# Kernel tuning notes

Measured on AMD Instinct MI355X. Metric: run time of the kernel, lower is better.

The kernel has to match this reference:

```python
import jax, jax.numpy as jnp
import numpy as np

NUM_ROUTES = 12800   # 32 * 20 * 20
NUM_CAPS = 25
IN_CH = 8
OUT_CH = 64
BATCH = 8
NUM_ITERS = 3


def setup_inputs() -> dict:
    key = jax.random.key(0)
    kx, kw = jax.random.split(key)
    x = jax.random.normal(kx, (BATCH, NUM_ROUTES, IN_CH), dtype=jnp.float32)
    # W parameter: torch shape [1, R, C, O, I] -> store as [R, C, O, I]
    W = jax.random.normal(kw, (NUM_ROUTES, NUM_CAPS, OUT_CH, IN_CH), dtype=jnp.float32)
    return {"x": x, "W": W}


def _squash_elementwise(s):
    # Faithful to source: squared_norm sums over last dim of s_j which has size 1,
    # so squash acts elementwise: s^2 * s / ((1+s^2) * |s|) = s*|s|/(1+s^2).
    sq = s * s
    return sq * s / ((1.0 + sq) * jnp.sqrt(sq))


def reference(x, W):
    # u_hat[b,r,c,o] = sum_i W[r,c,o,i] * x[b,r,i]
    u_hat = jnp.einsum('rcoi,bri->brco', W, x)  # [B, R, C, O]
    b_ij = jnp.zeros((NUM_ROUTES, NUM_CAPS), dtype=x.dtype)
    v = None
    for it in range(NUM_ITERS):
        # legacy F.softmax on 4D [1,R,C,1] uses implicit dim=1 -> over routes
        c_ij = jax.nn.softmax(b_ij, axis=0)                  # [R, C]
        s = jnp.einsum('rc,brco->bco', c_ij, u_hat)          # [B, C, O]
        v = _squash_elementwise(s)
        if it < NUM_ITERS - 1:
            # agreement: <u_hat, v> per (b,r,c), then mean over batch
            a = jnp.einsum('brco,bco->brc', u_hat, v)
            b_ij = b_ij + jnp.mean(a, axis=0)
    # torch returns v_j.squeeze(1) with shape [B, C, O, 1]
    return v[..., None]
```

## Files before the change

kernel.cpp:

```cpp
#include <hip/hip_runtime.h>
#include <cstdint>
#include <cstddef>

#define RN 12800
#define CN 25
#define ON 64
#define IN_ 8
#define BN 8
#define SOUT (BN*CN*ON)

#define RPC 64
#define NRC (RN / RPC)

template<int MODE>
__global__ void __launch_bounds__(320, 6)
caps_pass(const float* __restrict__ x, const float* __restrict__ W,
          const float* __restrict__ vin, const float* __restrict__ bin,
          float* __restrict__ bout, float* __restrict__ Sp, float* __restrict__ Zp)
{
    __shared__ float xs[RPC][BN][IN_];

    const int chunk = blockIdx.y;
    const int r0 = chunk * RPC;

    for (int t = threadIdx.x; t < RPC * BN * 2; t += 320) {
        const int i4 = t & 1;
        const int rl = (t >> 1) & (RPC - 1);
        const int b  = t >> 7;
        const float4 val = *reinterpret_cast<const float4*>(
            x + (((size_t)b * RN + r0 + rl) * IN_) + i4 * 4);
        *reinterpret_cast<float4*>(&xs[rl][b][i4 * 4]) = val;
    }
    __syncthreads();

    const int wave = threadIdx.x >> 6;
    const int lane = threadIdx.x & 63;
    const int c = blockIdx.x * 5 + wave;

    float acc[BN];
    #pragma unroll
    for (int b = 0; b < BN; ++b) acc[b] = 0.f;

    float vreg[BN];
    if (MODE >= 1) {
        #pragma unroll
        for (int b = 0; b < BN; ++b)
            vreg[b] = vin[(b * CN + c) * ON + lane];
    }
    float zacc = 0.f;

    #pragma unroll 2
    for (int rl = 0; rl < RPC; ++rl) {
        const int r = r0 + rl;
        const float4* wp = reinterpret_cast<const float4*>(
            W + ((((size_t)r * CN + c) * ON + lane) * IN_));
        const float4 w0 = wp[0];
        const float4 w1 = wp[1];

        float u[BN];
        #pragma unroll
        for (int b = 0; b < BN; ++b) {
            const float4 xa = *reinterpret_cast<const float4*>(&xs[rl][b][0]);
            const float4 xb = *reinterpret_cast<const float4*>(&xs[rl][b][4]);
            u[b] = w0.x*xa.x + w0.y*xa.y + w0.z*xa.z + w0.w*xa.w
                 + w1.x*xb.x + w1.y*xb.y + w1.z*xb.z + w1.w*xb.w;
        }

        if (MODE == 0) {
            #pragma unroll
            for (int b = 0; b < BN; ++b) acc[b] += u[b];
        } else {
            float p = 0.f;
            #pragma unroll
            for (int b = 0; b < BN; ++b) p += u[b] * vreg[b];
            #pragma unroll
            for (int off = 32; off > 0; off >>= 1) p += __shfl_xor(p, off, 64);
            float bn = p * (1.0f / BN);
            if (MODE == 2) bn += bin[(size_t)r * CN + c];
            if (MODE == 1 && lane == 0) bout[(size_t)r * CN + c] = bn;
            const float e = __expf(bn);
            zacc += e;
            #pragma unroll
            for (int b = 0; b < BN; ++b) acc[b] += e * u[b];
        }
    }

    float* sp = Sp + (size_t)chunk * SOUT;
    #pragma unroll
    for (int b = 0; b < BN; ++b)
        sp[(b * CN + c) * ON + lane] = acc[b];
    if (MODE >= 1 && lane == 0)
        Zp[chunk * 32 + c] = zacc;
}

template<int PASS>
__global__ void caps_finalize(const float* __restrict__ Sp, const float* __restrict__ Zp,
                              float* __restrict__ vout)
{
    const int idx = blockIdx.x * blockDim.x + threadIdx.x;
    if (idx >= SOUT) return;
    const int c = (idx >> 6) % CN;
    float s = 0.f;
    for (int w = 0; w < NRC; ++w) s += Sp[(size_t)w * SOUT + idx];
    float z;
    if (PASS == 0) {
        z = (float)RN;
    } else {
        z = 0.f;
        for (int w = 0; w < NRC; ++w) z += Zp[w * 32 + c];
    }
    s /= z;
    vout[idx] = s * fabsf(s) / (1.f + s * s);
}

extern "C" void kernel_launch(void* const* d_in, const int* in_sizes, int n_in,
                              void* d_out, int out_size, void* d_ws, size_t ws_size,
                              hipStream_t stream)
{
    const float* x = (const float*)d_in[0];
    const float* W = (const float*)d_in[1];
    float* out = (float*)d_out;
    float* ws = (float*)d_ws;

    float* v  = ws;
    float* b1 = ws + SOUT;
    float* Zp = b1 + (size_t)RN * CN;
    float* Sp = Zp + (size_t)NRC * 32;

    dim3 blk(320), grid(5, NRC);
    dim3 fblk(256), fgrid((SOUT + 255) / 256);

    caps_pass<0><<<grid, blk, 0, stream>>>(x, W, nullptr, nullptr, nullptr, Sp, Zp);
    caps_finalize<0><<<fgrid, fblk, 0, stream>>>(Sp, Zp, v);
    caps_pass<1><<<grid, blk, 0, stream>>>(x, W, v, nullptr, b1, Sp, Zp);
    caps_finalize<1><<<fgrid, fblk, 0, stream>>>(Sp, Zp, v);
    caps_pass<2><<<grid, blk, 0, stream>>>(x, W, v, b1, nullptr, Sp, Zp);
    caps_finalize<2><<<fgrid, fblk, 0, stream>>>(Sp, Zp, out);
}
```

Baseline: 435.4 us.

## Cache u_hat as packed bf16 and reuse it in routing passes

The first pass computes u_hat from W and x and also writes it to workspace as bf16, eight batch values packed per lane. The two routing passes then read this 12800x25x64x8 bf16 buffer (about 328 MB) instead of re-reading W in fp32 (about 655 MB) and redoing the matvec. The finalize step now splits the partial-sum reduction across four thread groups, and the normalizer sum is precomputed once per pass by a new small kernel. In exchange it adds a large bf16 write in the first pass and bf16 rounding error in the agreement and weighted-sum terms.

Result: faster. 384.1 us (-11.8%).

```diff
diff --git a/kernel.cpp b/kernel.cpp
--- a/kernel.cpp
+++ b/kernel.cpp
@@ -12,14 +12,21 @@
 #define RPC 64
 #define NRC (RN / RPC)
 
-template<int MODE>
+__device__ __forceinline__ uint32_t pack_bf16(float a, float b) {
+    uint32_t ua = __float_as_uint(a);
+    uint32_t ub = __float_as_uint(b);
+    ua = (ua + 0x7fffu + ((ua >> 16) & 1u)) >> 16;
+    ub = (ub + 0x7fffu + ((ub >> 16) & 1u)) & 0xffff0000u;
+    return ua | ub;
+}
+__device__ __forceinline__ float lo_bf16(uint32_t q) { return __uint_as_float(q << 16); }
+__device__ __forceinline__ float hi_bf16(uint32_t q) { return __uint_as_float(q & 0xffff0000u); }
+
 __global__ void __launch_bounds__(320, 6)
-caps_pass(const float* __restrict__ x, const float* __restrict__ W,
-          const float* __restrict__ vin, const float* __restrict__ bin,
-          float* __restrict__ bout, float* __restrict__ Sp, float* __restrict__ Zp)
+caps_pass0(const float* __restrict__ x, const float* __restrict__ W,
+           float* __restrict__ Sp, uint32_t* __restrict__ U)
 {
     __shared__ float xs[RPC][BN][IN_];
-
     const int chunk = blockIdx.y;
     const int r0 = chunk * RPC;
 
@@ -41,14 +48,6 @@
     #pragma unroll
     for (int b = 0; b < BN; ++b) acc[b] = 0.f;
 
-    float vreg[BN];
-    if (MODE >= 1) {
-        #pragma unroll
-        for (int b = 0; b < BN; ++b)
-            vreg[b] = vin[(b * CN + c) * ON + lane];
-    }
-    float zacc = 0.f;
-
     #pragma unroll 2
     for (int rl = 0; rl < RPC; ++rl) {
         const int r = r0 + rl;
@@ -64,53 +63,120 @@
             const float4 xb = *reinterpret_cast<const float4*>(&xs[rl][b][4]);
             u[b] = w0.x*xa.x + w0.y*xa.y + w0.z*xa.z + w0.w*xa.w
                  + w1.x*xb.x + w1.y*xb.y + w1.z*xb.z + w1.w*xb.w;
+            acc[b] += u[b];
         }
 
-        if (MODE == 0) {
-            #pragma unroll
-            for (int b = 0; b < BN; ++b) acc[b] += u[b];
-        } else {
-            float p = 0.f;
-            #pragma unroll
-            for (int b = 0; b < BN; ++b) p += u[b] * vreg[b];
-            #pragma unroll
-            for (int off = 32; off > 0; off >>= 1) p += __shfl_xor(p, off, 64);
-            float bn = p * (1.0f / BN);
-            if (MODE == 2) bn += bin[(size_t)r * CN + c];
-            if (MODE == 1 && lane == 0) bout[(size_t)r * CN + c] = bn;
-            const float e = __expf(bn);
-            zacc += e;
-            #pragma unroll
-            for (int b = 0; b < BN; ++b) acc[b] += e * u[b];
-        }
+        uint4 q;
+        q.x = pack_bf16(u[0], u[1]);
+        q.y = pack_bf16(u[2], u[3]);
+        q.z = pack_bf16(u[4], u[5]);
+        q.w = pack_bf16(u[6], u[7]);
+        *reinterpret_cast<uint4*>(U + (((size_t)r * CN + c) * ON + lane) * 4) = q;
     }
 
     float* sp = Sp + (size_t)chunk * SOUT;
     #pragma unroll
     for (int b = 0; b < BN; ++b)
         sp[(b * CN + c) * ON + lane] = acc[b];
-    if (MODE >= 1 && lane == 0)
+}
+
+template<int MODE>
+__global__ void __launch_bounds__(320, 6)
+caps_passU(const uint32_t* __restrict__ U, const float* __restrict__ vin,
+           const float* __restrict__ bin, float* __restrict__ bout,
+           float* __restrict__ Sp, float* __restrict__ Zp)
+{
+    const int chunk = blockIdx.y;
+    const int r0 = chunk * RPC;
+    const int wave = threadIdx.x >> 6;
+    const int lane = threadIdx.x & 63;
+    const int c = blockIdx.x * 5 + wave;
+
+    float vreg[BN];
+    #pragma unroll
+    for (int b = 0; b < BN; ++b)
+        vreg[b] = vin[(b * CN + c) * ON + lane];
+
+    float acc[BN];
+    #pragma unroll
+    for (int b = 0; b < BN; ++b) acc[b] = 0.f;
+    float zacc = 0.f;
+
+    #pragma unroll 2
+    for (int rl = 0; rl < RPC; ++rl) {
+        const int r = r0 + rl;
+        const uint4 q = *reinterpret_cast<const uint4*>(
+            U + (((size_t)r * CN + c) * ON + lane) * 4);
+        float u[BN];
+        u[0] = lo_bf16(q.x); u[1] = hi_bf16(q.x);
+        u[2] = lo_bf16(q.y); u[3] = hi_bf16(q.y);
+        u[4] = lo_bf16(q.z); u[5] = hi_bf16(q.z);
+        u[6] = lo_bf16(q.w); u[7] = hi_bf16(q.w);
+
+        float p = 0.f;
+        #pragma unroll
+        for (int b = 0; b < BN; ++b) p += u[b] * vreg[b];
+        #pragma unroll
+        for (int off = 32; off > 0; off >>= 1) p += __shfl_xor(p, off, 64);
+
+        float bn = p * (1.0f / BN);
+        if (MODE == 2) bn += bin[(size_t)r * CN + c];
+        if (MODE == 1 && lane == 0) bout[(size_t)r * CN + c] = bn;
+        const float e = __expf(bn);
+        zacc += e;
+        #pragma unroll
+        for (int b = 0; b < BN; ++b) acc[b] += e * u[b];
+    }
+
+    float* sp = Sp + (size_t)chunk * SOUT;
+    #pragma unroll
+    for (int b = 0; b < BN; ++b)
+        sp[(b * CN + c) * ON + lane] = acc[b];
+    if (lane == 0)
         Zp[chunk * 32 + c] = zacc;
 }
 
+__global__ void caps_zred(const float* __restrict__ Zp, float* __restrict__ z)
+{
+    __shared__ float l[256];
+    const int t = threadIdx.x;
+    const int cc = t >> 3;
+    const int g  = t & 7;
+    float s = 0.f;
+    if (cc < CN)
+        for (int j = g; j < NRC; j += 8) s += Zp[j * 32 + cc];
+    l[t] = s;
+    __syncthreads();
+    if (g == 0 && cc < CN) {
+        float ss = 0.f;
+        #pragma unroll
+        for (int k = 0; k < 8; ++k) ss += l[cc * 8 + k];
+        z[cc] = ss;
+    }
+}
+
 template<int PASS>
-__global__ void caps_finalize(const float* __restrict__ Sp, const float* __restrict__ Zp,
-                              float* __restrict__ vout)
-{
-    const int idx = blockIdx.x * blockDim.x + threadIdx.x;
-    if (idx >= SOUT) return;
-    const int c = (idx >> 6) % CN;
+__global__ void __launch_bounds__(256)
+caps_fin(const float* __restrict__ Sp, const float* __restrict__ z,
+         float* __restrict__ vout)
+{
+    __shared__ float l[256];
+    const int blk = blockIdx.x;
+    const int t = threadIdx.x;
+    const int o = t & 63;
+    const int g = t >> 6;
+    const int base = blk * 64 + o;
     float s = 0.f;
-    for (int w = 0; w < NRC; ++w) s += Sp[(size_t)w * SOUT + idx];
-    float z;
-    if (PASS == 0) {
-        z = (float)RN;
-    } else {
-        z = 0.f;
-        for (int w = 0; w < NRC; ++w) z += Zp[w * 32 + c];
-    }
-    s /= z;
-    vout[idx] = s * fabsf(s) / (1.f + s * s);
+    for (int w = g * 50; w < g * 50 + 50; ++w)
+        s += Sp[(size_t)w * SOUT + base];
+    l[t] = s;
+    __syncthreads();
+    if (g == 0) {
+        float ss = l[o] + l[64 + o] + l[128 + o] + l[192 + o];
+        const float zz = (PASS == 0) ? (float)RN : z[blk % CN];
+        ss /= zz;
+        vout[base] = ss * fabsf(ss) / (1.f + ss * ss);
+    }
 }
 
 extern "C" void kernel_launch(void* const* d_in, const int* in_sizes, int n_in,
@@ -123,17 +189,21 @@
     float* ws = (float*)d_ws;
 
     float* v  = ws;
-    float* b1 = ws + SOUT;
+    float* z  = v + SOUT;
+    float* b1 = z + 32;
     float* Zp = b1 + (size_t)RN * CN;
     float* Sp = Zp + (size_t)NRC * 32;
+    uint32_t* U = (uint32_t*)(Sp + (size_t)NRC * SOUT);
 
     dim3 blk(320), grid(5, NRC);
-    dim3 fblk(256), fgrid((SOUT + 255) / 256);
-
-    caps_pass<0><<<grid, blk, 0, stream>>>(x, W, nullptr, nullptr, nullptr, Sp, Zp);
-    caps_finalize<0><<<fgrid, fblk, 0, stream>>>(Sp, Zp, v);
-    caps_pass<1><<<grid, blk, 0, stream>>>(x, W, v, nullptr, b1, Sp, Zp);
-    caps_finalize<1><<<fgrid, fblk, 0, stream>>>(Sp, Zp, v);
-    caps_pass<2><<<grid, blk, 0, stream>>>(x, W, v, b1, nullptr, Sp, Zp);
-    caps_finalize<2><<<fgrid, fblk, 0, stream>>>(Sp, Zp, out);
-}
+    dim3 fblk(256), fgrid(BN * CN);
+
+    caps_pass0<<<grid, blk, 0, stream>>>(x, W, Sp, U);
+    caps_fin<0><<<fgrid, fblk, 0, stream>>>(Sp, z, v);
+    caps_passU<1><<<grid, blk, 0, stream>>>(U, v, nullptr, b1, Sp, Zp);
+    caps_zred<<<1, 256, 0, stream>>>(Zp, z);
+    caps_fin<1><<<fgrid, fblk, 0, stream>>>(Sp, z, v);
+    caps_passU<2><<<grid, blk, 0, stream>>>(U, v, b1, nullptr, Sp, Zp);
+    caps_zred<<<1, 256, 0, stream>>>(Zp, z);
+    caps_fin<2><<<fgrid, fblk, 0, stream>>>(Sp, z, out);
+}
```
